# Kernel optimization log

Measured on AMD Instinct MI355X. Metric: run time of the kernel, lower is better.

## Reference

```python
import jax, jax.numpy as jnp
import numpy as np

U = 100000          # unique pillars
N = 2 * U           # voxels (2 per pillar -> unq_cnt==2, mask all True)
NUM_BINS = 32       # z bins
C_IN = 5
C_HID = 32          # out_channels // 2 in conv1d MLP
C_OUT = 64
R = 4               # channel-attention reduction
K = 7               # bin-attention conv kernel


def setup_inputs() -> dict:
    key = jax.random.key(0)
    ks = jax.random.split(key, 12)
    voxel_features = jax.random.normal(ks[0], (N, C_IN), jnp.float32)
    # each pillar p owns voxels 2p, 2p+1 placed in two distinct bins -> no scatter collision
    bins = (jnp.arange(N, dtype=jnp.int32) % NUM_BINS)
    voxel_coords = jnp.zeros((N, 4), jnp.int32).at[:, 1].set(bins)
    unq_coords = jnp.arange(U, dtype=jnp.int32)
    unq_inv = jnp.arange(N, dtype=jnp.int32) // 2
    unq_cnt = jnp.full((U,), 2, jnp.int32)
    s = 0.3
    return {
        'voxel_features': voxel_features,
        'voxel_coords': voxel_coords,
        'unq_coords': unq_coords,
        'unq_inv': unq_inv,
        'unq_cnt': unq_cnt,
        # up_dimension MLP (Linear(5,32) -> relu -> Linear(32,64))
        'W1': jax.random.normal(ks[1], (C_IN, C_HID), jnp.float32) * s,
        'b1': jnp.zeros((C_HID,), jnp.float32),
        'W2': jax.random.normal(ks[2], (C_HID, C_OUT), jnp.float32) * s,
        'b2': jnp.zeros((C_OUT,), jnp.float32),
        # ZBAM channel-attention shared MLP
        'Wc1': jax.random.normal(ks[3], (C_OUT, C_OUT // R), jnp.float32) * s,
        'bc1': jnp.zeros((C_OUT // R,), jnp.float32),
        'Wc2': jax.random.normal(ks[4], (C_OUT // R, C_OUT), jnp.float32) * s,
        'bc2': jnp.zeros((C_OUT,), jnp.float32),
        # ZBAM bin (spatial) attention: conv1d over bins, 2->1 channels, kernel 7
        'Wsp': jax.random.normal(ks[5], (1, 2, K), jnp.float32) * s,
        'bsp': jnp.zeros((1,), jnp.float32),
    }


def _cbam_forward(voxel_features, W1, b1, W2, b2, Wc1, bc1, Wc2, bc2, Wsp, bsp,
                  voxel_coords, unq_coords, unq_inv, unq_cnt):
    n_pillars = unq_coords.shape[0]
    # --- binning: scatter voxels into (pillar, z-bin) slots ---
    src = jnp.zeros((n_pillars, NUM_BINS, voxel_features.shape[1]), voxel_features.dtype)
    src = src.at[unq_inv, voxel_coords[:, 1]].set(voxel_features)
    occupied_mask = unq_cnt >= 2  # all True by construction -> src[mask] == src
    # --- up_dimension MLP: (U, bins, 5) -> (U, bins, 64) ---
    x = jax.nn.relu(src @ W1 + b1) @ W2 + b2
    x = jnp.transpose(x, (0, 2, 1))  # (U, C, bins)
    # --- ZBAM channel attention ---
    avg_p = x.mean(axis=2)
    max_p = x.max(axis=2)
    mlp = lambda v: jax.nn.relu(v @ Wc1 + bc1) @ Wc2 + bc2
    att_c = jax.nn.sigmoid(mlp(avg_p) + mlp(max_p))  # (U, C)
    x = x * att_c[:, :, None]
    # --- ZBAM bin attention (conv over z-bins) ---
    s = jnp.stack([x.mean(axis=1), x.max(axis=1)], axis=1)  # (U, 2, bins)
    att_s = jax.lax.conv_general_dilated(
        s, Wsp, window_strides=(1,), padding=[(K // 2, K // 2)],
        dimension_numbers=('NCH', 'OIH', 'NCH')) + bsp  # (U, 1, bins)
    x = x * jax.nn.sigmoid(att_s)
    # --- max-pool over bins ---
    return x.max(axis=2), occupied_mask


def reference(voxel_features, voxel_coords, unq_coords, unq_inv, unq_cnt,
              W1, b1, W2, b2, Wc1, bc1, Wc2, bc2, Wsp, bsp):
    return _cbam_forward(voxel_features, W1, b1, W2, b2, Wc1, bc1, Wc2, bc2,
                         Wsp, bsp, voxel_coords, unq_coords, unq_inv, unq_cnt)
```

## Files before the change

kernel.cpp:

```cpp
#include <hip/hip_runtime.h>
#include <math.h>


#define CO 64

typedef __attribute__((ext_vector_type(8))) short s16x8;
typedef __attribute__((ext_vector_type(4))) float f32x4;
union ABu { uint4 u4; s16x8 s; };

__device__ __forceinline__ float sgm(float x) {
  return 1.0f / (1.0f + __expf(-x));
}
template <int PAT>
__device__ __forceinline__ float qadd(float s) {
  int t = __builtin_amdgcn_update_dpp(0, __builtin_bit_cast(int, s),
                                      PAT, 0xf, 0xf, true);
  return s + __builtin_bit_cast(float, t);
}
template <int PAT>
__device__ __forceinline__ float qmaxd(float m) {
  int t = __builtin_amdgcn_update_dpp(__builtin_bit_cast(int, m),
                                      __builtin_bit_cast(int, m),
                                      PAT, 0xf, 0xf, false);
  return fmaxf(m, __builtin_bit_cast(float, t));
}
template <int PAT>
__device__ __forceinline__ float qmind(float m) {
  int t = __builtin_amdgcn_update_dpp(__builtin_bit_cast(int, m),
                                      __builtin_bit_cast(int, m),
                                      PAT, 0xf, 0xf, false);
  return fminf(m, __builtin_bit_cast(float, t));
}
__device__ __forceinline__ float qsum4(float s) { return qadd<0x4E>(qadd<0xB1>(s)); }
__device__ __forceinline__ float qmax4(float m) { return qmaxd<0x4E>(qmaxd<0xB1>(m)); }
__device__ __forceinline__ float qmin4(float m) { return qmind<0x4E>(qmind<0xB1>(m)); }
__device__ __forceinline__ void drain_lds() {
  __builtin_amdgcn_wave_barrier();
  __builtin_amdgcn_s_waitcnt(0xC07F);
  __builtin_amdgcn_wave_barrier();
}
__device__ __forceinline__ void drain_vm() {
  __builtin_amdgcn_wave_barrier();
  __builtin_amdgcn_s_waitcnt(0x0F70);
  __builtin_amdgcn_wave_barrier();
}

__device__ __forceinline__ uint rtn16(float f) {
  uint u = __builtin_bit_cast(uint, f);
  return u + 0x7fffu + ((u >> 16) & 1u);
}
__device__ __forceinline__ uint cvtpk(float a, float b) {
  uint r;
  asm("v_cvt_pk_bf16_f32 %0, %1, %2" : "=v"(r) : "v"(a), "v"(b));
  return r;
}
__device__ __forceinline__ void mk_frag(const float* e, ABu& hi, ABu& lo) {
  uint h[4], l[4];
#pragma unroll
  for (int p = 0; p < 4; ++p) {
    h[p] = cvtpk(e[2 * p], e[2 * p + 1]);
    float d0 = e[2 * p]     - __builtin_bit_cast(float, h[p] << 16);
    float d1 = e[2 * p + 1] - __builtin_bit_cast(float, h[p] & 0xffff0000u);
    l[p] = cvtpk(d0, d1);
  }
  hi.u4 = make_uint4(h[0], h[1], h[2], h[3]);
  lo.u4 = make_uint4(l[0], l[1], l[2], l[3]);
}

__global__ __launch_bounds__(256) void pack_kernel(
    const float* __restrict__ vf, const int* __restrict__ vcoord,
    const int* __restrict__ unq_inv, float* __restrict__ pvox, int n) {
  int i = blockIdx.x * blockDim.x + threadIdx.x;
  if (i >= n) return;
  int p = unq_inv[i];
  int slot = (i > 0 && unq_inv[i - 1] == p) ? 1 : 0;
  float* dst = pvox + 8 * (size_t)(2 * p + slot);
#pragma unroll
  for (int k = 0; k < 5; ++k) dst[k] = vf[5 * i + k];
  ((int*)dst)[5] = vcoord[4 * i + 1];
}

__global__ __launch_bounds__(256) void cbam_kernel(
    const float* __restrict__ pvox, const int* __restrict__ unq_cnt,
    const float* __restrict__ W1, const float* __restrict__ b1,
    const float* __restrict__ W2, const float* __restrict__ b2,
    const float* __restrict__ Wc1, const float* __restrict__ bc1,
    const float* __restrict__ Wc2, const float* __restrict__ bc2,
    const float* __restrict__ Wsp, const float* __restrict__ bsp,
    float* __restrict__ out, int U, int ngroups, int totalWaves) {
  __shared__ __align__(16) uint4 w2fh[256], w2fl[256];
  __shared__ __align__(16) uint4 wc1fh[128], wc1fl[128];
  __shared__ __align__(16) float w1b[160], b1b[32];
  __shared__ __align__(16) float wc2b[1024];
  __shared__ __align__(16) float c0b[64], b2b[64], bc2b[64], bc1b[16];
  __shared__ __align__(16) float wsmx[64];
  __shared__ __align__(16) float wtab[16];
  __shared__ __align__(16) float vbuf[4][256];
  __shared__ __align__(16) float ybuf[4][1088];

  const int tid = threadIdx.x;

  {
    const int nt = tid >> 6, l = tid & 63, gg = l >> 4, cc = l & 15;
    uint hu[4], lu[4];
#pragma unroll
    for (int p = 0; p < 4; ++p) {
      float f0 = W2[(8 * gg + 2 * p)     * 64 + 16 * nt + cc];
      float f1 = W2[(8 * gg + 2 * p + 1) * 64 + 16 * nt + cc];
      uint r0 = rtn16(f0), r1 = rtn16(f1);
      hu[p] = (r0 >> 16) | (r1 & 0xffff0000u);
      float d0 = f0 - __builtin_bit_cast(float, r0 & 0xffff0000u);
      float d1 = f1 - __builtin_bit_cast(float, r1 & 0xffff0000u);
      uint s0 = rtn16(d0), s1 = rtn16(d1);
      lu[p] = (s0 >> 16) | (s1 & 0xffff0000u);
    }
    w2fh[tid] = make_uint4(hu[0], hu[1], hu[2], hu[3]);
    w2fl[tid] = make_uint4(lu[0], lu[1], lu[2], lu[3]);
  }
  if (tid < 128) {
    const int ks = tid >> 6, l = tid & 63, gg = l >> 4, cc = l & 15;
    uint hu[4], lu[4];
#pragma unroll
    for (int p = 0; p < 4; ++p) {
      float f0 = Wc1[(32 * ks + 8 * gg + 2 * p)     * 16 + cc];
      float f1 = Wc1[(32 * ks + 8 * gg + 2 * p + 1) * 16 + cc];
      uint r0 = rtn16(f0), r1 = rtn16(f1);
      hu[p] = (r0 >> 16) | (r1 & 0xffff0000u);
      float d0 = f0 - __builtin_bit_cast(float, r0 & 0xffff0000u);
      float d1 = f1 - __builtin_bit_cast(float, r1 & 0xffff0000u);
      uint s0 = rtn16(d0), s1 = rtn16(d1);
      lu[p] = (s0 >> 16) | (s1 & 0xffff0000u);
    }
    wc1fh[tid] = make_uint4(hu[0], hu[1], hu[2], hu[3]);
    wc1fl[tid] = make_uint4(lu[0], lu[1], lu[2], lu[3]);
  }
  if (tid < 160) w1b[tid] = W1[tid];
  if (tid < 32) b1b[tid] = b1[tid];
  for (int i = tid; i < 1024; i += 256) {
    int ch = i >> 4, j = i & 15, qq = ch >> 4, k = ch & 15;
    wc2b[(4 * k + qq) * 16 + j] = Wc2[j * 64 + ch];
  }
  if (tid < 64) { b2b[tid] = b2[tid]; bc2b[tid] = bc2[tid]; }
  if (tid < 16) bc1b[tid] = bc1[tid];
  if (tid < 32) {
    float sm = 0.0f, sx = 0.0f;
    for (int k = 0; k < 7; ++k)
      if ((unsigned)(tid + k - 3) < 32u) { sm += Wsp[k]; sx += Wsp[7 + k]; }
    wsmx[2 * tid] = sm; wsmx[2 * tid + 1] = sx;
  }
  if (tid < 8) {
    float a = 0.0f, b = 0.0f;
    if (tid < 7) { a = Wsp[tid]; b = Wsp[7 + tid]; }
    wtab[2 * tid] = a; wtab[2 * tid + 1] = b;
  }
  __syncthreads();
  if (tid < 64) {
    float c = b2b[tid];
    for (int j = 0; j < 32; ++j) c += fmaxf(b1b[j], 0.0f) * W2[j * 64 + tid];
    c0b[tid] = c;
  }
  __syncthreads();

  const int wv = tid >> 6, lane = tid & 63;
  int grp = blockIdx.x * 4 + wv;
  if (grp >= ngroups) return;

  float* const vb = vbuf[wv];
  float4* const vb4 = (float4*)vb;
  float* const scr = ybuf[wv];
  float4* const yb4 = (float4*)scr;
  float2* const yb2 = (float2*)scr;

  const int c16 = lane & 15, g = lane >> 4;
  const int q = lane & 3, pp = lane >> 2;
  const float4* pv4 = (const float4*)pvox;
  const int f4max = 4 * U - 1;

  {
    int idx = 64 * grp + lane;
    idx = idx < f4max ? idx : f4max;
    __builtin_amdgcn_global_load_lds(
        (const __attribute__((address_space(1))) void*)(pv4 + idx),
        (__attribute__((address_space(3))) void*)vb4, 16, 0, 0);
  }
  drain_vm();

  for (; grp < ngroups; grp += totalWaves) {
    int ofs0 = 0;
    asm volatile("" : "+s"(ofs0));

    const int P0 = grp * 16;

    const int pg = P0 + pp;
    const int pc = pg < U ? pg : (U - 1);
    const int cnt = unq_cnt[pc];
    const int* vbi = (const int*)vb;
    const int b0 = vbi[(2 * pp) * 8 + 5] & 31;
    const int b1raw = vbi[(2 * pp + 1) * 8 + 5];

    ABu ah0, al0, ah1, al1;
    {
      const float4* vb4c = (const float4*)vb;
      float4 xa = vb4c[2 * c16], xb = vb4c[2 * c16 + 1];
      float4 yc = vb4c[2 * (c16 + 16)], yd = vb4c[2 * (c16 + 16) + 1];
      float va[5] = {xa.x, xa.y, xa.z, xa.w, xb.x};
      float vc[5] = {yc.x, yc.y, yc.z, yc.w, yd.x};
      const float4* w1b4 = (const float4*)w1b;
      const float4* b1b4 = (const float4*)b1b;
      float4 bA = b1b4[ofs0 + 2 * g], bB = b1b4[ofs0 + 2 * g + 1];
      float e0[8] = {bA.x, bA.y, bA.z, bA.w, bB.x, bB.y, bB.z, bB.w};
      float e1[8] = {bA.x, bA.y, bA.z, bA.w, bB.x, bB.y, bB.z, bB.w};
#pragma unroll
      for (int d = 0; d < 5; ++d) {
        float4 w0 = w1b4[ofs0 + d * 8 + 2 * g];
        float4 w1v = w1b4[ofs0 + d * 8 + 2 * g + 1];
        e0[0] += va[d] * w0.x;  e0[1] += va[d] * w0.y;
        e0[2] += va[d] * w0.z;  e0[3] += va[d] * w0.w;
        e0[4] += va[d] * w1v.x; e0[5] += va[d] * w1v.y;
        e0[6] += va[d] * w1v.z; e0[7] += va[d] * w1v.w;
        e1[0] += vc[d] * w0.x;  e1[1] += vc[d] * w0.y;
        e1[2] += vc[d] * w0.z;  e1[3] += vc[d] * w0.w;
        e1[4] += vc[d] * w1v.x; e1[5] += vc[d] * w1v.y;
        e1[6] += vc[d] * w1v.z; e1[7] += vc[d] * w1v.w;
      }
#pragma unroll
      for (int i = 0; i < 8; ++i) {
        e0[i] = fmaxf(e0[i], 0.0f);
        e1[i] = fmaxf(e1[i], 0.0f);
      }
      mk_frag(e0, ah0, al0);
      mk_frag(e1, ah1, al1);
    }
    drain_lds();

    {
      const int nxt = grp + totalWaves;
      if (nxt < ngroups) {
        int nidx = 64 * nxt + lane;
        nidx = nidx < f4max ? nidx : f4max;
        __builtin_amdgcn_global_load_lds(
            (const __attribute__((address_space(1))) void*)(pv4 + nidx),
            (__attribute__((address_space(3))) void*)vb4, 16, 0, 0);
      }
    }

    float y0[16], y1[16];
#pragma unroll
    for (int nt = 0; nt < 4; ++nt) {
      ABu bh, bl;
      bh.u4 = w2fh[ofs0 + nt * 64 + lane];
      bl.u4 = w2fl[ofs0 + nt * 64 + lane];
      f32x4 acc[2];
      acc[0] = 0; acc[1] = 0;
      acc[0] = __builtin_amdgcn_mfma_f32_16x16x32_bf16(ah0.s, bh.s, acc[0], 0, 0, 0);
      acc[0] = __builtin_amdgcn_mfma_f32_16x16x32_bf16(al0.s, bh.s, acc[0], 0, 0, 0);
      acc[0] = __builtin_amdgcn_mfma_f32_16x16x32_bf16(ah0.s, bl.s, acc[0], 0, 0, 0);
      acc[0] = __builtin_amdgcn_mfma_f32_16x16x32_bf16(al0.s, bl.s, acc[0], 0, 0, 0);
      acc[1] = __builtin_amdgcn_mfma_f32_16x16x32_bf16(ah1.s, bh.s, acc[1], 0, 0, 0);
      acc[1] = __builtin_amdgcn_mfma_f32_16x16x32_bf16(al1.s, bh.s, acc[1], 0, 0, 0);
      acc[1] = __builtin_amdgcn_mfma_f32_16x16x32_bf16(ah1.s, bl.s, acc[1], 0, 0, 0);
      acc[1] = __builtin_amdgcn_mfma_f32_16x16x32_bf16(al1.s, bl.s, acc[1], 0, 0, 0);
      const float b2v = b2b[16 * nt + c16];
#pragma unroll
      for (int mt = 0; mt < 2; ++mt)
#pragma unroll
        for (int rp = 0; rp < 2; ++rp) {
          const int p = 8 * mt + 2 * g + rp;
          float2 v2;
          v2.x = acc[mt][2 * rp]     + b2v;
          v2.y = acc[mt][2 * rp + 1] + b2v;
          yb2[p * 18 + c16] = v2;
        }
      if (q == nt) {
#pragma unroll
        for (int kk = 0; kk < 8; ++kk) {
          float4 t = yb4[pp * 9 + kk];
          y0[2 * kk]     = t.x; y1[2 * kk]     = t.y;
          y0[2 * kk + 1] = t.z; y1[2 * kk + 1] = t.w;
        }
      }
    }

    const bool has2 = (cnt >= 2);
    const int b1e = has2 ? (b1raw & 31) : 64;
#pragma unroll
    for (int k = 0; k < 16; ++k) y1[k] = has2 ? y1[k] : y0[k];

    float gq[16];
    {
      const float kf = has2 ? 30.0f : 31.0f;
      const float inv32 = 1.0f / 32.0f;
      const float4* c04 = (const float4*)c0b;
#pragma unroll
      for (int kb = 0; kb < 4; ++kb) {
        float4 cq = c04[q * 4 + kb];
        float4 t;
        t.x = fmaf(cq.x, kf, y0[4 * kb + 0] + (has2 ? y1[4 * kb + 0] : 0.0f)) * inv32;
        t.y = fmaf(cq.y, kf, y0[4 * kb + 1] + (has2 ? y1[4 * kb + 1] : 0.0f)) * inv32;
        t.z = fmaf(cq.z, kf, y0[4 * kb + 2] + (has2 ? y1[4 * kb + 2] : 0.0f)) * inv32;
        t.w = fmaf(cq.w, kf, y0[4 * kb + 3] + (has2 ? y1[4 * kb + 3] : 0.0f)) * inv32;
        *((float4*)(scr + pp * 68 + 16 * q) + kb) = t;
      }
      ABu ah[2], al[2];
#pragma unroll
      for (int ks = 0; ks < 2; ++ks) {
        const float4* s4 = (const float4*)(scr + c16 * 68 + 32 * ks + 8 * g);
        float4 p0 = s4[0], p1 = s4[1];
        float e[8] = {p0.x, p0.y, p0.z, p0.w, p1.x, p1.y, p1.z, p1.w};
        mk_frag(e, ah[ks], al[ks]);
      }
      f32x4 accA = 0;
#pragma unroll
      for (int ks = 0; ks < 2; ++ks) {
        ABu bh, bl;
        bh.u4 = wc1fh[ofs0 + ks * 64 + lane];
        bl.u4 = wc1fl[ofs0 + ks * 64 + lane];
        accA = __builtin_amdgcn_mfma_f32_16x16x32_bf16(ah[ks].s, bh.s, accA, 0, 0, 0);
        accA = __builtin_amdgcn_mfma_f32_16x16x32_bf16(al[ks].s, bh.s, accA, 0, 0, 0);
        accA = __builtin_amdgcn_mfma_f32_16x16x32_bf16(ah[ks].s, bl.s, accA, 0, 0, 0);
        accA = __builtin_amdgcn_mfma_f32_16x16x32_bf16(al[ks].s, bl.s, accA, 0, 0, 0);
      }
#pragma unroll
      for (int kb = 0; kb < 4; ++kb) {
        float4 cq = c04[q * 4 + kb];
        float4 t;
        t.x = fmaxf(fmaxf(y0[4 * kb + 0], y1[4 * kb + 0]), cq.x);
        t.y = fmaxf(fmaxf(y0[4 * kb + 1], y1[4 * kb + 1]), cq.y);
        t.z = fmaxf(fmaxf(y0[4 * kb + 2], y1[4 * kb + 2]), cq.z);
        t.w = fmaxf(fmaxf(y0[4 * kb + 3], y1[4 * kb + 3]), cq.w);
        *((float4*)(scr + pp * 68 + 16 * q) + kb) = t;
      }
#pragma unroll
      for (int ks = 0; ks < 2; ++ks) {
        const float4* s4 = (const float4*)(scr + c16 * 68 + 32 * ks + 8 * g);
        float4 p0 = s4[0], p1 = s4[1];
        float e[8] = {p0.x, p0.y, p0.z, p0.w, p1.x, p1.y, p1.z, p1.w};
        mk_frag(e, ah[ks], al[ks]);
      }
      f32x4 accM = 0;
#pragma unroll
      for (int ks = 0; ks < 2; ++ks) {
        ABu bh, bl;
        bh.u4 = wc1fh[ofs0 + ks * 64 + lane];
        bl.u4 = wc1fl[ofs0 + ks * 64 + lane];
        accM = __builtin_amdgcn_mfma_f32_16x16x32_bf16(ah[ks].s, bh.s, accM, 0, 0, 0);
        accM = __builtin_amdgcn_mfma_f32_16x16x32_bf16(al[ks].s, bh.s, accM, 0, 0, 0);
        accM = __builtin_amdgcn_mfma_f32_16x16x32_bf16(ah[ks].s, bl.s, accM, 0, 0, 0);
        accM = __builtin_amdgcn_mfma_f32_16x16x32_bf16(al[ks].s, bl.s, accM, 0, 0, 0);
      }
      const float bc1v = bc1b[c16];
#pragma unroll
      for (int r = 0; r < 4; ++r) {
        const float gv = fmaxf(accA[r] + bc1v, 0.0f) +
                         fmaxf(accM[r] + bc1v, 0.0f);
        scr[(4 * g + r) * 20 + c16] = gv;
      }
      const float4* g4 = (const float4*)(scr + pp * 20);
#pragma unroll
      for (int jb = 0; jb < 4; ++jb) {
        float4 t = g4[jb];
        gq[4 * jb] = t.x; gq[4 * jb + 1] = t.y;
        gq[4 * jb + 2] = t.z; gq[4 * jb + 3] = t.w;
      }
    }

    const float4* c04 = (const float4*)c0b;
    float attc[16];
    float sc = 0.0f, mc = -3.0e38f;
    float sy0 = 0.0f, my0 = -3.0e38f, sy1 = 0.0f, my1 = -3.0e38f;
    const float4* wc24 = (const float4*)wc2b;
    const float4* bc24 = (const float4*)bc2b;
#pragma unroll
    for (int kb = 0; kb < 4; ++kb) {
      float4 cq = c04[q * 4 + kb];
      float4 bq = bc24[q * 4 + kb];
      float c0a[4] = {cq.x, cq.y, cq.z, cq.w};
      float b2a[4] = {bq.x, bq.y, bq.z, bq.w};
#pragma unroll
      for (int i = 0; i < 4; ++i) {
        const int k = 4 * kb + i;
        float pre = 2.0f * b2a[i];
#pragma unroll
        for (int jb = 0; jb < 4; ++jb) {
          float4 w = wc24[(4 * k + q) * 4 + jb];
          pre += gq[4 * jb] * w.x + gq[4 * jb + 1] * w.y +
                 gq[4 * jb + 2] * w.z + gq[4 * jb + 3] * w.w;
        }
        const float a = sgm(pre);
        attc[k] = a;
        const float pc0 = a * c0a[i], py0 = a * y0[k], py1 = a * y1[k];
        sc += pc0;  mc = fmaxf(mc, pc0);
        sy0 += py0; my0 = fmaxf(my0, py0);
        sy1 += py1; my1 = fmaxf(my1, py1);
      }
    }
    sc = qsum4(sc);   mc = qmax4(mc);
    sy0 = qsum4(sy0); my0 = qmax4(my0);
    sy1 = qsum4(sy1); my1 = qmax4(my1);

    const float inv64 = 1.0f / 64.0f;
    const float Mn = sc * inv64, Mx = mc;
    const float dm0 = (sy0 - sc) * inv64, dx0 = my0 - mc;
    const float dm1 = (sy1 - sc) * inv64, dx1 = my1 - mc;
    const float bspr = bsp[0];
    const float2* ws2 = (const float2*)wsmx;
    const float2* wt2 = (const float2*)wtab;
    float maxE = -3.0e38f, minE = 3.0e38f, sv0 = -3.0e38f, sv1 = -3.0e38f;
#pragma unroll
    for (int k = 0; k < 8; ++k) {
      const int b = 8 * q + k;
      float2 ws = ws2[b];
      float acc2 = bspr + Mn * ws.x + Mx * ws.y;
      int k0 = b0 - b + 3;  k0 = ((unsigned)k0 <= 6u) ? k0 : 7;
      int k1 = b1e - b + 3; k1 = ((unsigned)k1 <= 6u) ? k1 : 7;
      float2 w0 = wt2[k0];
      float2 w1v = wt2[k1];
      acc2 += dm0 * w0.x + dx0 * w0.y + dm1 * w1v.x + dx1 * w1v.y;
      const bool o0 = (b == b0), o1 = (b == b1e);
      const bool oc = o0 || o1;
      maxE = fmaxf(maxE, oc ? -3.0e38f : acc2);
      minE = fminf(minE, oc ?  3.0e38f : acc2);
      sv0 = o0 ? acc2 : sv0;
      sv1 = o1 ? acc2 : sv1;
    }
    maxE = qmax4(maxE); minE = qmin4(minE);
    sv0 = qmax4(sv0);   sv1 = qmax4(sv1);
    const float sig0 = sgm(sv0);
    const float sig1 = has2 ? sgm(sv1) : sig0;
    const float sE = sgm(maxE), sI = sgm(minE);

    if (pg < U) {
      float4* ov = (float4*)(out + (size_t)pg * CO + 16 * q);
#pragma unroll
      for (int kb = 0; kb < 4; ++kb) {
        float4 cq = c04[q * 4 + kb];
        float c0a[4] = {cq.x, cq.y, cq.z, cq.w};
        float rr[4];
#pragma unroll
        for (int i = 0; i < 4; ++i) {
          const int k = 4 * kb + i;
          const float c0v = c0a[i];
          const float sel = (c0v >= 0.0f) ? sE : sI;
          const float m = fmaxf(fmaxf(y0[k] * sig0, y1[k] * sig1), c0v * sel);
          rr[i] = attc[k] * m;
        }
        float4 r; r.x = rr[0]; r.y = rr[1]; r.z = rr[2]; r.w = rr[3];
        ov[kb] = r;
      }
      if (q == 0) out[(size_t)U * CO + pg] = has2 ? 1.0f : 0.0f;
    }

    drain_vm();
  }
}

extern "C" void kernel_launch(void* const* d_in, const int* in_sizes, int n_in,
                              void* d_out, int out_size, void* d_ws, size_t ws_size,
                              hipStream_t stream) {
  const float* vf      = (const float*)d_in[0];
  const int*   vcoord  = (const int*)d_in[1];
  const int*   unq_inv = (const int*)d_in[3];
  const int*   unq_cnt = (const int*)d_in[4];
  const float* W1  = (const float*)d_in[5];
  const float* b1  = (const float*)d_in[6];
  const float* W2  = (const float*)d_in[7];
  const float* b2  = (const float*)d_in[8];
  const float* Wc1 = (const float*)d_in[9];
  const float* bc1 = (const float*)d_in[10];
  const float* Wc2 = (const float*)d_in[11];
  const float* bc2 = (const float*)d_in[12];
  const float* Wsp = (const float*)d_in[13];
  const float* bsp = (const float*)d_in[14];

  const int N = in_sizes[3];
  const int U = in_sizes[4];

  float* pvox = (float*)d_ws;

  pack_kernel<<<(N + 255) / 256, 256, 0, stream>>>(vf, vcoord, unq_inv, pvox, N);

  static int blocksPerCU = 0;
  if (blocksPerCU == 0) {
    hipFuncAttributes a{};
    blocksPerCU = 4;
    if (hipFuncGetAttributes(&a, (const void*)cbam_kernel) == hipSuccess) {
      int byV = 4;
      if (a.numRegs > 0) {
        if (a.numRegs <= 64) byV = 8;
        else if (a.numRegs <= 128) byV = 4;
        else byV = 2;
      }
      int byL = (a.sharedSizeBytes > 0)
                    ? (int)(163840 / (int)a.sharedSizeBytes) : 4;
      int m = byV < byL ? byV : byL;
      if (m < 1) m = 1;
      if (m > 8) m = 8;
      blocksPerCU = m;
    }
  }

  const int ngroups = (U + 15) / 16;
  int blocks = 256 * blocksPerCU;
  const int maxBlocks = (ngroups + 3) / 4;
  if (blocks > maxBlocks) blocks = maxBlocks;
  const int totalWaves = blocks * 4;
  cbam_kernel<<<blocks, 256, 0, stream>>>(
      pvox, unq_cnt, W1, b1, W2, b2, Wc1, bc1, Wc2, bc2, Wsp, bsp,
      (float*)d_out, U, ngroups, totalWaves);
}
```

Measured before the change: 130.7 us.

## Move channel-attention second layer to split-bf16 MFMA and drop lo*lo terms

Replaces the scalar FMA evaluation of the Wc2 layer (per-thread dot products read from LDS) with a split-bf16 MFMA over the concatenated avg/max hidden activations. Wc2 is pre-split into hi/lo bf16 fragments in shared memory, and the sigmoid results are staged through scratch LDS. It also drops the lo*lo MFMA term in every split-bf16 product, cutting matrix instructions by a quarter. The cost is slightly lower precision and some extra LDS round trips.

```diff
diff --git a/kernel.cpp b/kernel.cpp
--- a/kernel.cpp
+++ b/kernel.cpp
@@ -90,8 +90,8 @@
     float* __restrict__ out, int U, int ngroups, int totalWaves) {
   __shared__ __align__(16) uint4 w2fh[256], w2fl[256];
   __shared__ __align__(16) uint4 wc1fh[128], wc1fl[128];
+  __shared__ __align__(16) uint4 wc2fh[128], wc2fl[128];
   __shared__ __align__(16) float w1b[160], b1b[32];
-  __shared__ __align__(16) float wc2b[1024];
   __shared__ __align__(16) float c0b[64], b2b[64], bc2b[64], bc1b[16];
   __shared__ __align__(16) float wsmx[64];
   __shared__ __align__(16) float wtab[16];
@@ -134,12 +134,25 @@
     wc1fh[tid] = make_uint4(hu[0], hu[1], hu[2], hu[3]);
     wc1fl[tid] = make_uint4(lu[0], lu[1], lu[2], lu[3]);
   }
+  if (tid < 128) {
+    const int nt = tid >> 5, r5 = tid & 31, g01 = r5 >> 4, cc = r5 & 15;
+    uint hu[4], lu[4];
+#pragma unroll
+    for (int p = 0; p < 4; ++p) {
+      float f0 = Wc2[(8 * g01 + 2 * p)     * 64 + 16 * nt + cc];
+      float f1 = Wc2[(8 * g01 + 2 * p + 1) * 64 + 16 * nt + cc];
+      uint r0 = rtn16(f0), r1 = rtn16(f1);
+      hu[p] = (r0 >> 16) | (r1 & 0xffff0000u);
+      float d0 = f0 - __builtin_bit_cast(float, r0 & 0xffff0000u);
+      float d1 = f1 - __builtin_bit_cast(float, r1 & 0xffff0000u);
+      uint s0 = rtn16(d0), s1 = rtn16(d1);
+      lu[p] = (s0 >> 16) | (s1 & 0xffff0000u);
+    }
+    wc2fh[tid] = make_uint4(hu[0], hu[1], hu[2], hu[3]);
+    wc2fl[tid] = make_uint4(lu[0], lu[1], lu[2], lu[3]);
+  }
   if (tid < 160) w1b[tid] = W1[tid];
   if (tid < 32) b1b[tid] = b1[tid];
-  for (int i = tid; i < 1024; i += 256) {
-    int ch = i >> 4, j = i & 15, qq = ch >> 4, k = ch & 15;
-    wc2b[(4 * k + qq) * 16 + j] = Wc2[j * 64 + ch];
-  }
   if (tid < 64) { b2b[tid] = b2[tid]; bc2b[tid] = bc2[tid]; }
   if (tid < 16) bc1b[tid] = bc1[tid];
   if (tid < 32) {
@@ -255,11 +268,9 @@
       acc[0] = __builtin_amdgcn_mfma_f32_16x16x32_bf16(ah0.s, bh.s, acc[0], 0, 0, 0);
       acc[0] = __builtin_amdgcn_mfma_f32_16x16x32_bf16(al0.s, bh.s, acc[0], 0, 0, 0);
       acc[0] = __builtin_amdgcn_mfma_f32_16x16x32_bf16(ah0.s, bl.s, acc[0], 0, 0, 0);
-      acc[0] = __builtin_amdgcn_mfma_f32_16x16x32_bf16(al0.s, bl.s, acc[0], 0, 0, 0);
       acc[1] = __builtin_amdgcn_mfma_f32_16x16x32_bf16(ah1.s, bh.s, acc[1], 0, 0, 0);
       acc[1] = __builtin_amdgcn_mfma_f32_16x16x32_bf16(al1.s, bh.s, acc[1], 0, 0, 0);
       acc[1] = __builtin_amdgcn_mfma_f32_16x16x32_bf16(ah1.s, bl.s, acc[1], 0, 0, 0);
-      acc[1] = __builtin_amdgcn_mfma_f32_16x16x32_bf16(al1.s, bl.s, acc[1], 0, 0, 0);
       const float b2v = b2b[16 * nt + c16];
 #pragma unroll
       for (int mt = 0; mt < 2; ++mt)
@@ -286,7 +297,7 @@
 #pragma unroll
     for (int k = 0; k < 16; ++k) y1[k] = has2 ? y1[k] : y0[k];
 
-    float gq[16];
+    f32x4 accA = 0, accM = 0;
     {
       const float kf = has2 ? 30.0f : 31.0f;
       const float inv32 = 1.0f / 32.0f;
@@ -309,7 +320,6 @@
         float e[8] = {p0.x, p0.y, p0.z, p0.w, p1.x, p1.y, p1.z, p1.w};
         mk_frag(e, ah[ks], al[ks]);
       }
-      f32x4 accA = 0;
 #pragma unroll
       for (int ks = 0; ks < 2; ++ks) {
         ABu bh, bl;
@@ -318,7 +328,6 @@
         accA = __builtin_amdgcn_mfma_f32_16x16x32_bf16(ah[ks].s, bh.s, accA, 0, 0, 0);
         accA = __builtin_amdgcn_mfma_f32_16x16x32_bf16(al[ks].s, bh.s, accA, 0, 0, 0);
         accA = __builtin_amdgcn_mfma_f32_16x16x32_bf16(ah[ks].s, bl.s, accA, 0, 0, 0);
-        accA = __builtin_amdgcn_mfma_f32_16x16x32_bf16(al[ks].s, bl.s, accA, 0, 0, 0);
       }
 #pragma unroll
       for (int kb = 0; kb < 4; ++kb) {
@@ -337,7 +346,6 @@
         float e[8] = {p0.x, p0.y, p0.z, p0.w, p1.x, p1.y, p1.z, p1.w};
         mk_frag(e, ah[ks], al[ks]);
       }
-      f32x4 accM = 0;
 #pragma unroll
       for (int ks = 0; ks < 2; ++ks) {
         ABu bh, bl;
@@ -346,48 +354,63 @@
         accM = __builtin_amdgcn_mfma_f32_16x16x32_bf16(ah[ks].s, bh.s, accM, 0, 0, 0);
         accM = __builtin_amdgcn_mfma_f32_16x16x32_bf16(al[ks].s, bh.s, accM, 0, 0, 0);
         accM = __builtin_amdgcn_mfma_f32_16x16x32_bf16(ah[ks].s, bl.s, accM, 0, 0, 0);
-        accM = __builtin_amdgcn_mfma_f32_16x16x32_bf16(al[ks].s, bl.s, accM, 0, 0, 0);
-      }
+      }
+    }
+
+    float attc[16];
+    {
       const float bc1v = bc1b[c16];
 #pragma unroll
       for (int r = 0; r < 4; ++r) {
-        const float gv = fmaxf(accA[r] + bc1v, 0.0f) +
-                         fmaxf(accM[r] + bc1v, 0.0f);
-        scr[(4 * g + r) * 20 + c16] = gv;
-      }
-      const float4* g4 = (const float4*)(scr + pp * 20);
-#pragma unroll
-      for (int jb = 0; jb < 4; ++jb) {
-        float4 t = g4[jb];
-        gq[4 * jb] = t.x; gq[4 * jb + 1] = t.y;
-        gq[4 * jb + 2] = t.z; gq[4 * jb + 3] = t.w;
+        scr[(4 * g + r) * 36 + c16]      = fmaxf(accA[r] + bc1v, 0.0f);
+        scr[(4 * g + r) * 36 + 16 + c16] = fmaxf(accM[r] + bc1v, 0.0f);
+      }
+      ABu a2h, a2l;
+      {
+        const float4* s4 = (const float4*)(scr + c16 * 36 + 8 * g);
+        float4 p0 = s4[0], p1 = s4[1];
+        float e[8] = {p0.x, p0.y, p0.z, p0.w, p1.x, p1.y, p1.z, p1.w};
+        mk_frag(e, a2h, a2l);
+      }
+      f32x4 acc2[4];
+#pragma unroll
+      for (int nt = 0; nt < 4; ++nt) {
+        ABu bh, bl;
+        bh.u4 = wc2fh[ofs0 + nt * 32 + (g & 1) * 16 + c16];
+        bl.u4 = wc2fl[ofs0 + nt * 32 + (g & 1) * 16 + c16];
+        f32x4 a = 0;
+        a = __builtin_amdgcn_mfma_f32_16x16x32_bf16(a2h.s, bh.s, a, 0, 0, 0);
+        a = __builtin_amdgcn_mfma_f32_16x16x32_bf16(a2l.s, bh.s, a, 0, 0, 0);
+        a = __builtin_amdgcn_mfma_f32_16x16x32_bf16(a2h.s, bl.s, a, 0, 0, 0);
+        acc2[nt] = a;
+      }
+#pragma unroll
+      for (int nt = 0; nt < 4; ++nt) {
+        const float b2c = 2.0f * bc2b[16 * nt + c16];
+#pragma unroll
+        for (int r = 0; r < 4; ++r)
+          scr[(4 * g + r) * 68 + 16 * nt + c16] = sgm(acc2[nt][r] + b2c);
+      }
+      const float4* a4 = (const float4*)(scr + pp * 68 + 16 * q);
+#pragma unroll
+      for (int kb = 0; kb < 4; ++kb) {
+        float4 t = a4[kb];
+        attc[4 * kb] = t.x; attc[4 * kb + 1] = t.y;
+        attc[4 * kb + 2] = t.z; attc[4 * kb + 3] = t.w;
       }
     }
 
     const float4* c04 = (const float4*)c0b;
-    float attc[16];
     float sc = 0.0f, mc = -3.0e38f;
     float sy0 = 0.0f, my0 = -3.0e38f, sy1 = 0.0f, my1 = -3.0e38f;
-    const float4* wc24 = (const float4*)wc2b;
-    const float4* bc24 = (const float4*)bc2b;
 #pragma unroll
     for (int kb = 0; kb < 4; ++kb) {
       float4 cq = c04[q * 4 + kb];
-      float4 bq = bc24[q * 4 + kb];
       float c0a[4] = {cq.x, cq.y, cq.z, cq.w};
-      float b2a[4] = {bq.x, bq.y, bq.z, bq.w};
 #pragma unroll
       for (int i = 0; i < 4; ++i) {
         const int k = 4 * kb + i;
-        float pre = 2.0f * b2a[i];
-#pragma unroll
-        for (int jb = 0; jb < 4; ++jb) {
-          float4 w = wc24[(4 * k + q) * 4 + jb];
-          pre += gq[4 * jb] * w.x + gq[4 * jb + 1] * w.y +
-                 gq[4 * jb + 2] * w.z + gq[4 * jb + 3] * w.w;
-        }
-        const float a = sgm(pre);
-        attc[k] = a;
+        const float a = attc[k];
         const float pc0 = a * c0a[i], py0 = a * y0[k], py1 = a * y1[k];
         sc += pc0;  mc = fmaxf(mc, pc0);
         sy0 += py0; my0 = fmaxf(my0, py0);
@@ -410,18 +433,18 @@
     for (int k = 0; k < 8; ++k) {
       const int b = 8 * q + k;
       float2 ws = ws2[b];
-      float acc2 = bspr + Mn * ws.x + Mx * ws.y;
+      float acc2v = bspr + Mn * ws.x + Mx * ws.y;
       int k0 = b0 - b + 3;  k0 = ((unsigned)k0 <= 6u) ? k0 : 7;
       int k1 = b1e - b + 3; k1 = ((unsigned)k1 <= 6u) ? k1 : 7;
       float2 w0 = wt2[k0];
       float2 w1v = wt2[k1];
-      acc2 += dm0 * w0.x + dx0 * w0.y + dm1 * w1v.x + dx1 * w1v.y;
+      acc2v += dm0 * w0.x + dx0 * w0.y + dm1 * w1v.x + dx1 * w1v.y;
       const bool o0 = (b == b0), o1 = (b == b1e);
       const bool oc = o0 || o1;
-      maxE = fmaxf(maxE, oc ? -3.0e38f : acc2);
-      minE = fminf(minE, oc ?  3.0e38f : acc2);
-      sv0 = o0 ? acc2 : sv0;
-      sv1 = o1 ? acc2 : sv1;
+      maxE = fmaxf(maxE, oc ? -3.0e38f : acc2v);
+      minE = fminf(minE, oc ?  3.0e38f : acc2v);
+      sv0 = o0 ? acc2v : sv0;
+      sv1 = o1 ? acc2v : sv1;
     }
     maxE = qmax4(maxE); minE = qmin4(minE);
     sv0 = qmax4(sv0);   sv1 = qmax4(sv1);
```

After: 125.5 us. 1.04x faster.
